# Performance work log

Hardware: AMD Instinct MI355X
Metric: run time of the kernel (lower is better)

Reference implementation:

```python
import jax, jax.numpy as jnp
import numpy as np

B, T, D = 2, 2048, 2048
NH, NKV, HD = 16, 4, 128
EPS = 1e-6
ROPE_THETA = 10000.0


def rms_norm(x, w):
    # per-head RMSNorm over the last (head_dim) axis
    var = jnp.mean(jnp.square(x), axis=-1, keepdims=True)
    return x * jax.lax.rsqrt(var + EPS) * w


def rope_sin_cos(seq_len, dim, dtype):
    inv_freq = 1.0 / (ROPE_THETA ** (jnp.arange(0, dim, 2, dtype=jnp.float32) / dim))
    t = jnp.arange(seq_len, dtype=jnp.float32)
    ang = jnp.outer(t, inv_freq)                      # [T, HD/2]
    ang = jnp.concatenate([ang, ang], axis=-1)         # [T, HD]
    return jnp.sin(ang).astype(dtype), jnp.cos(ang).astype(dtype)


def rotate_half(x):
    x1, x2 = jnp.split(x, 2, axis=-1)
    return jnp.concatenate([-x2, x1], axis=-1)


def apply_rope(x, sin, cos):
    # x: [B, T, H, HD]; sin/cos: [T, HD]
    s = sin[None, :, None, :]
    c = cos[None, :, None, :]
    return x * c + rotate_half(x) * s


def setup_inputs() -> dict:
    key = jax.random.key(0)
    ks = jax.random.split(key, 5)
    scale = 1.0 / np.sqrt(D)
    return {
        "x": jax.random.normal(ks[0], (B, T, D), jnp.float32),
        "wq": jax.random.normal(ks[1], (D, D), jnp.float32) * scale,
        "wk": jax.random.normal(ks[2], (NKV * HD, D), jnp.float32) * scale,
        "wv": jax.random.normal(ks[3], (NKV * HD, D), jnp.float32) * scale,
        "wo": jax.random.normal(ks[4], (D, D), jnp.float32) * scale,
        "q_norm_w": jnp.ones((HD,), jnp.float32),
        "k_norm_w": jnp.ones((HD,), jnp.float32),
    }


def reference(x, wq, wk, wv, wo, q_norm_w, k_norm_w):
    b, t, _ = x.shape
    q = (x @ wq.T).reshape(b, t, NH, HD)    # [B,T,NH,HD]
    k = (x @ wk.T).reshape(b, t, NKV, HD)   # [B,T,NKV,HD]
    v = (x @ wv.T).reshape(b, t, NKV, HD)

    # per-head QK RMS norm
    q = rms_norm(q, q_norm_w)
    k = rms_norm(k, k_norm_w)

    # RoPE
    sin, cos = rope_sin_cos(t, HD, x.dtype)
    q = apply_rope(q, sin, cos)
    k = apply_rope(k, sin, cos)

    # GQA: expand kv heads to match query heads
    rep = NH // NKV
    k = jnp.repeat(k, rep, axis=2)          # [B,T,NH,HD]
    v = jnp.repeat(v, rep, axis=2)

    # causal SDPA
    scale = 1.0 / np.sqrt(HD)
    scores = jnp.einsum('bqhd,bkhd->bhqk', q, k) * scale
    causal = jnp.tril(jnp.ones((t, t), bool))
    scores = jnp.where(causal[None, None], scores, jnp.finfo(scores.dtype).min)
    probs = jax.nn.softmax(scores, axis=-1)
    att = jnp.einsum('bhqk,bkhd->bqhd', probs, v).reshape(b, t, NH * HD)
    return att @ wo.T
```

## Files before the change

### kernel.cpp

```cpp
#include <hip/hip_runtime.h>
#include <hip/hip_bf16.h>

#define B_ 2
#define T_ 2048
#define D_ 2048
#define NH_ 16
#define NKV_ 4
#define HD_ 128

using bf16 = __bf16;
using bf16x8 = __attribute__((ext_vector_type(8))) __bf16;
using bf16x4 = __attribute__((ext_vector_type(4))) __bf16;
using f32x4 = __attribute__((ext_vector_type(4))) float;

__device__ __forceinline__ void gld_lds16(bf16* lds, const bf16* g) {
  __builtin_amdgcn_global_load_lds(
      (const __attribute__((address_space(1))) void*)g,
      (__attribute__((address_space(3))) void*)lds, 16, 0, 0);
}

__global__ __launch_bounds__(256) void cvt_bf16(const float* __restrict__ in,
                                                bf16* __restrict__ out, int n4) {
  int i = blockIdx.x * 256 + threadIdx.x;
  if (i >= n4) return;
  float4 v = ((const float4*)in)[i];
  bf16x4 o;
  o[0] = (bf16)v.x; o[1] = (bf16)v.y; o[2] = (bf16)v.z; o[3] = (bf16)v.w;
  ((bf16x4*)out)[i] = o;
}

template<typename OutT>
__global__ __launch_bounds__(256) void gemm_bt(const bf16* __restrict__ A,
                                               const bf16* __restrict__ Bt,
                                               OutT* __restrict__ C,
                                               int M, int N, int K) {
  __shared__ bf16 As[128 * 32];
  __shared__ bf16 Bs[128 * 32];
  const int tid = threadIdx.x;
  const int wid = tid >> 6;
  const int lane = tid & 63;
  const int g = lane >> 4, r = lane & 15;
  const int wm = wid >> 1, wn = wid & 1;
  const int gx = gridDim.x;
  const int nwg = gx * gridDim.y;
  const int flat = blockIdx.y * gx + blockIdx.x;
  const int swz = (flat & 7) * (nwg >> 3) + (flat >> 3);
  const long bm = (long)(swz / gx) * 128, bn = (long)(swz % gx) * 128;
  f32x4 acc[4][4] = {};

  for (int k0 = 0; k0 < K; k0 += 32) {
    __syncthreads();
    for (int c = 0; c < 2; ++c) {
      int ch = wid * 2 + c;
      int row = ch * 16 + (lane >> 2);
      int col = (lane & 3) * 8;
      gld_lds16(As + ch * 512, A + (bm + row) * K + k0 + col);
      gld_lds16(Bs + ch * 512, Bt + (bn + row) * K + k0 + col);
    }
    asm volatile("s_waitcnt vmcnt(0)" ::: "memory");
    __syncthreads();
    bf16x8 af[4], bfr[4];
    for (int m = 0; m < 4; ++m)
      af[m] = *(const bf16x8*)(As + (wm * 64 + m * 16 + r) * 32 + g * 8);
    for (int n = 0; n < 4; ++n)
      bfr[n] = *(const bf16x8*)(Bs + (wn * 64 + n * 16 + r) * 32 + g * 8);
    for (int m = 0; m < 4; ++m)
      for (int n = 0; n < 4; ++n)
        acc[m][n] = __builtin_amdgcn_mfma_f32_16x16x32_bf16(af[m], bfr[n], acc[m][n], 0, 0, 0);
  }

  for (int m = 0; m < 4; ++m)
    for (int n = 0; n < 4; ++n)
      for (int e = 0; e < 4; ++e) {
        long row = bm + wm * 64 + m * 16 + g * 4 + e;
        long col = bn + wn * 64 + n * 16 + r;
        C[row * N + col] = (OutT)acc[m][n][e];
      }
}

template<int IS_K>
__global__ __launch_bounds__(256) void norm_rope(const bf16* __restrict__ qkv,
                                                 const float* __restrict__ w,
                                                 bf16* __restrict__ out) {
  const int lane = threadIdx.x & 63;
  const int rloc = threadIdx.x >> 6;
  const int NHH = IS_K ? NKV_ : NH_;
  const int COFF = IS_K ? 2048 : 0;
  const long rid = (long)blockIdx.x * 4 + rloc;
  const int h = (int)(rid % NHH);
  const long bt = rid / NHH;
  const int t = (int)(bt % T_);
  const bf16* src = qkv + bt * 3072 + COFF + h * HD_;
  float v0 = (float)src[lane];
  float v1 = (float)src[lane + 64];
  float ss = v0 * v0 + v1 * v1;
  for (int o = 1; o < 64; o <<= 1) ss += __shfl_xor(ss, o, 64);
  float inv = rsqrtf(ss * (1.f / HD_) + 1e-6f);
  float n0 = v0 * inv * w[lane];
  float n1 = v1 * inv * w[lane + 64];
  float ang = (float)t * exp2f((float)lane * (-13.287712379549449f / 64.f));
  float sv, cv;
  __sincosf(ang, &sv, &cv);
  float o0 = n0 * cv - n1 * sv;
  float o1 = n1 * cv + n0 * sv;
  bf16* dst;
  if (IS_K) {
    long b = bt / T_;
    dst = out + ((b * NKV_ + h) * (long)T_ + t) * HD_;
  } else {
    dst = out + (bt * NH_ + h) * HD_;
  }
  dst[lane] = (bf16)o0;
  dst[lane + 64] = (bf16)o1;
}

__global__ __launch_bounds__(256) void vpack(const bf16* __restrict__ qkv,
                                             bf16* __restrict__ Vt) {
  __shared__ float tile[64][65];
  const int tt = blockIdx.x;
  const int dd = blockIdx.y & 1;
  const int bkv = blockIdx.y >> 1;
  const long b = bkv >> 2;
  const int kv = bkv & 3;
  const int t0 = tt * 64, d0 = dd * 64;
  for (int i = 0; i < 2; ++i) {
    int row = i * 32 + (threadIdx.x >> 3);
    int c8 = (threadIdx.x & 7) * 8;
    bf16x8 v = *(const bf16x8*)&qkv[(b * T_ + t0 + row) * 3072 + 2560 + kv * HD_ + d0 + c8];
    for (int j = 0; j < 8; ++j) tile[row][c8 + j] = (float)v[j];
  }
  __syncthreads();
  for (int i = 0; i < 2; ++i) {
    int drow = i * 32 + (threadIdx.x >> 3);
    int tc8 = (threadIdx.x & 7) * 8;
    bf16x8 o;
    for (int j = 0; j < 8; ++j) o[j] = (bf16)tile[tc8 + j][drow];
    *(bf16x8*)&Vt[((b * NKV_ + kv) * (long)HD_ + d0 + drow) * T_ + t0 + tc8] = o;
  }
}

__global__ __launch_bounds__(512) void flash_attn(const bf16* __restrict__ Q,
                                                  const bf16* __restrict__ K,
                                                  const bf16* __restrict__ V,
                                                  bf16* __restrict__ O) {
  __shared__ bf16 Ks[2][64 * 128];
  __shared__ bf16 Vs[2][128 * 64];
  __shared__ bf16 Ps[8][16 * 64];
  const int qt = (gridDim.x - 1) - blockIdx.x;
  const int h = blockIdx.y, b = blockIdx.z;
  const int kv = h >> 2;
  const int tid = threadIdx.x, wid = tid >> 6, lane = tid & 63;
  const int g = lane >> 4, r = lane & 15;
  const int q0 = qt * 128;
  const int qbase = q0 + wid * 16;
  const int q = qbase + r;

  bf16x8 aq[4];
  const bf16* qp = Q + ((long)(b * T_ + q)) * (NH_ * HD_) + h * HD_;
  for (int kk = 0; kk < 4; ++kk) aq[kk] = *(const bf16x8*)(qp + kk * 32 + g * 8);

  f32x4 oacc[8] = {};
  float m_run = -1e30f, l_run = 0.f;

  const bf16* Kbase = K + ((long)(b * NKV_ + kv)) * T_ * HD_;
  const bf16* Vbase = V + ((long)(b * NKV_ + kv)) * (long)HD_ * T_;
  const int nkt = 2 * qt + 2;

  auto stageKV = [&](int buf, int k0) {
    for (int c = 0; c < 2; ++c) {
      int ch = wid * 2 + c;
      {
        int row = ch * 4 + (lane >> 4);
        int srccol = ((lane & 15) ^ (row & 7)) * 8;
        gld_lds16(&Ks[buf][ch * 512], Kbase + (long)(k0 + row) * HD_ + srccol);
      }
      {
        int row = ch * 8 + (lane >> 3);
        int srccol = ((lane & 7) ^ (row & 7)) * 8;
        gld_lds16(&Vs[buf][ch * 512], Vbase + (long)row * T_ + k0 + srccol);
      }
    }
  };

  stageKV(0, 0);
  for (int kt = 0; kt < nkt; ++kt) {
    const int k0 = kt * 64;
    const int cur = kt & 1;
    if (kt + 1 < nkt) {
      stageKV(cur ^ 1, k0 + 64);
      asm volatile("s_waitcnt vmcnt(4)" ::: "memory");
    } else {
      asm volatile("s_waitcnt vmcnt(0)" ::: "memory");
    }
    __builtin_amdgcn_s_barrier();

    f32x4 s[4] = {};
    __builtin_amdgcn_s_setprio(1);
    for (int n = 0; n < 4; ++n)
      for (int kk = 0; kk < 4; ++kk) {
        int row = n * 16 + r;
        bf16x8 bk = *(const bf16x8*)(&Ks[cur][row * 128 + (((kk * 4 + g) ^ (row & 7)) * 8)]);
        s[n] = __builtin_amdgcn_mfma_f32_16x16x32_bf16(bk, aq[kk], s[n], 0, 0, 0);
      }
    __builtin_amdgcn_s_setprio(0);

    const float scale = 0.088388347648318447f;
    const bool domask = (k0 + 63 > qbase);
    float mx = -1e30f;
    if (domask) {
      for (int n = 0; n < 4; ++n) {
        const int km = k0 + n * 16 + g * 4;
        for (int e = 0; e < 4; ++e) {
          float v = s[n][e] * scale;
          if (km + e > q) v = -1e30f;
          s[n][e] = v;
          mx = fmaxf(mx, v);
        }
      }
    } else {
      for (int n = 0; n < 4; ++n)
        for (int e = 0; e < 4; ++e) {
          float v = s[n][e] * scale;
          s[n][e] = v;
          mx = fmaxf(mx, v);
        }
    }
    mx = fmaxf(mx, __shfl_xor(mx, 16, 64));
    mx = fmaxf(mx, __shfl_xor(mx, 32, 64));
    float mnew = fmaxf(m_run, mx);
    float alpha = __expf(m_run - mnew);
    float ls = 0.f;
    for (int n = 0; n < 4; ++n) {
      bf16x4 pb;
      for (int e = 0; e < 4; ++e) {
        float p = __expf(s[n][e] - mnew);
        ls += p;
        pb[e] = (bf16)p;
      }
      int c = n * 2 + (g >> 1);
      *(bf16x4*)(&Ps[wid][r * 64 + ((c ^ (r & 7)) * 8) + (g & 1) * 4]) = pb;
    }
    ls += __shfl_xor(ls, 16, 64);
    ls += __shfl_xor(ls, 32, 64);
    m_run = mnew;
    l_run = l_run * alpha + ls;

    float al[4];
    for (int e = 0; e < 4; ++e)
      al[e] = __shfl(alpha, (lane & 48) | (g * 4 + e), 64);
    for (int dt = 0; dt < 8; ++dt)
      for (int e = 0; e < 4; ++e) oacc[dt][e] *= al[e];

    asm volatile("s_waitcnt lgkmcnt(0)" ::: "memory");

    __builtin_amdgcn_s_setprio(1);
    for (int kk = 0; kk < 2; ++kk) {
      bf16x8 ap = *(const bf16x8*)(&Ps[wid][r * 64 + (((kk * 4 + g) ^ (r & 7)) * 8)]);
      for (int dt = 0; dt < 8; ++dt) {
        int row = dt * 16 + r;
        bf16x8 bv = *(const bf16x8*)(&Vs[cur][row * 64 + (((kk * 4 + g) ^ (row & 7)) * 8)]);
        oacc[dt] = __builtin_amdgcn_mfma_f32_16x16x32_bf16(ap, bv, oacc[dt], 0, 0, 0);
      }
    }
    __builtin_amdgcn_s_setprio(0);
    __builtin_amdgcn_s_barrier();
  }

  float li[4];
  for (int e = 0; e < 4; ++e) {
    float lv = __shfl(l_run, (lane & 48) | (g * 4 + e), 64);
    li[e] = 1.f / lv;
  }
  for (int e = 0; e < 4; ++e) {
    const int grow = q0 + wid * 16 + g * 4 + e;
    bf16* dst = O + ((long)(b * T_ + grow)) * (NH_ * HD_) + h * HD_;
    for (int dt = 0; dt < 8; ++dt)
      dst[dt * 16 + r] = (bf16)(oacc[dt][e] * li[e]);
  }
}

extern "C" void kernel_launch(void* const* d_in, const int* in_sizes, int n_in,
                              void* d_out, int out_size, void* d_ws, size_t ws_size,
                              hipStream_t stream) {
  const float* x  = (const float*)d_in[0];
  const float* wq = (const float*)d_in[1];
  const float* wk = (const float*)d_in[2];
  const float* wv = (const float*)d_in[3];
  const float* wo = (const float*)d_in[4];
  const float* qw = (const float*)d_in[5];
  const float* kw = (const float*)d_in[6];
  float* out = (float*)d_out;

  char* p = (char*)d_ws;
  bf16* xb    = (bf16*)(p);
  bf16* wqkvb = (bf16*)(p + 16777216);
  bf16* wob   = (bf16*)(p + 29360128);
  bf16* QKVr  = (bf16*)(p + 37748736);
  bf16* Qb    = (bf16*)(p + 62914560);
  bf16* Kb    = (bf16*)(p + 79691776);
  bf16* Vt    = (bf16*)(p + 83886080);
  bf16* attb  = (bf16*)(p + 88080384);

  cvt_bf16<<<8192, 256, 0, stream>>>(x,  xb, 2097152);
  cvt_bf16<<<4096, 256, 0, stream>>>(wq, wqkvb,           1048576);
  cvt_bf16<<<1024, 256, 0, stream>>>(wk, wqkvb + 4194304,  262144);
  cvt_bf16<<<1024, 256, 0, stream>>>(wv, wqkvb + 5242880,  262144);
  cvt_bf16<<<4096, 256, 0, stream>>>(wo, wob, 1048576);

  gemm_bt<bf16><<<dim3(24, 32), 256, 0, stream>>>(xb, wqkvb, QKVr, 4096, 3072, 2048);

  norm_rope<0><<<16384, 256, 0, stream>>>(QKVr, qw, Qb);
  norm_rope<1><<<4096, 256, 0, stream>>>(QKVr, kw, Kb);
  vpack<<<dim3(32, 16), 256, 0, stream>>>(QKVr, Vt);

  flash_attn<<<dim3(16, 16, 2), 512, 0, stream>>>(Qb, Kb, Vt, attb);

  gemm_bt<float><<<dim3(16, 32), 256, 0, stream>>>(attb, wob, out, 4096, 2048, 2048);
}
```

Measured before the change: 256.1 us.

## Use exp2 softmax with lazy rescale and prefetch V fragments in flash attention

Folds log2(e) into the score scale so the softmax uses exp2f. Rescaling of the output accumulator is skipped unless some row max grows by more than 8 (in log2 units), which removes most of the per-tile multiplies. The first half of the V fragments is loaded from LDS before the softmax math so those reads overlap with the ALU work, and launch bounds now request 4 waves per SIMD. The cost is extra registers held across the softmax and possible spills under the tighter register bound, plus slightly larger intermediate exponent values from the lazy max.

```diff
diff --git a/kernel.cpp b/kernel.cpp
--- a/kernel.cpp
+++ b/kernel.cpp
@@ -139,10 +139,10 @@
   }
 }
 
-__global__ __launch_bounds__(512) void flash_attn(const bf16* __restrict__ Q,
-                                                  const bf16* __restrict__ K,
-                                                  const bf16* __restrict__ V,
-                                                  bf16* __restrict__ O) {
+__global__ __launch_bounds__(512, 4) void flash_attn(const bf16* __restrict__ Q,
+                                                     const bf16* __restrict__ K,
+                                                     const bf16* __restrict__ V,
+                                                     bf16* __restrict__ O) {
   __shared__ bf16 Ks[2][64 * 128];
   __shared__ bf16 Vs[2][128 * 64];
   __shared__ bf16 Ps[8][16 * 64];
@@ -204,14 +204,21 @@
       }
     __builtin_amdgcn_s_setprio(0);
 
-    const float scale = 0.088388347648318447f;
+    bf16x8 bva[8];
+    for (int dt = 0; dt < 8; ++dt) {
+      int row = dt * 16 + r;
+      bva[dt] = *(const bf16x8*)(&Vs[cur][row * 64 + ((g ^ (row & 7)) * 8)]);
+    }
+    __builtin_amdgcn_sched_barrier(0);
+
+    const float scale2 = 0.12751743f;
     const bool domask = (k0 + 63 > qbase);
     float mx = -1e30f;
     if (domask) {
       for (int n = 0; n < 4; ++n) {
         const int km = k0 + n * 16 + g * 4;
         for (int e = 0; e < 4; ++e) {
-          float v = s[n][e] * scale;
+          float v = s[n][e] * scale2;
           if (km + e > q) v = -1e30f;
           s[n][e] = v;
           mx = fmaxf(mx, v);
@@ -220,20 +227,20 @@
     } else {
       for (int n = 0; n < 4; ++n)
         for (int e = 0; e < 4; ++e) {
-          float v = s[n][e] * scale;
+          float v = s[n][e] * scale2;
           s[n][e] = v;
           mx = fmaxf(mx, v);
         }
     }
     mx = fmaxf(mx, __shfl_xor(mx, 16, 64));
     mx = fmaxf(mx, __shfl_xor(mx, 32, 64));
-    float mnew = fmaxf(m_run, mx);
-    float alpha = __expf(m_run - mnew);
+    const bool resc = !__all(mx <= m_run + 8.f);
+    const float mnew = resc ? fmaxf(m_run, mx) : m_run;
     float ls = 0.f;
     for (int n = 0; n < 4; ++n) {
       bf16x4 pb;
       for (int e = 0; e < 4; ++e) {
-        float p = __expf(s[n][e] - mnew);
+        float p = exp2f(s[n][e] - mnew);
         ls += p;
         pb[e] = (bf16)p;
       }
@@ -242,25 +249,34 @@
     }
     ls += __shfl_xor(ls, 16, 64);
     ls += __shfl_xor(ls, 32, 64);
-    m_run = mnew;
-    l_run = l_run * alpha + ls;
-
-    float al[4];
-    for (int e = 0; e < 4; ++e)
-      al[e] = __shfl(alpha, (lane & 48) | (g * 4 + e), 64);
-    for (int dt = 0; dt < 8; ++dt)
-      for (int e = 0; e < 4; ++e) oacc[dt][e] *= al[e];
+    if (resc) {
+      float alpha = exp2f(m_run - mnew);
+      float al[4];
+      for (int e = 0; e < 4; ++e)
+        al[e] = __shfl(alpha, (lane & 48) | (g * 4 + e), 64);
+      for (int dt = 0; dt < 8; ++dt)
+        for (int e = 0; e < 4; ++e) oacc[dt][e] *= al[e];
+      l_run = l_run * alpha + ls;
+      m_run = mnew;
+    } else {
+      l_run += ls;
+    }
 
     asm volatile("s_waitcnt lgkmcnt(0)" ::: "memory");
 
     __builtin_amdgcn_s_setprio(1);
-    for (int kk = 0; kk < 2; ++kk) {
-      bf16x8 ap = *(const bf16x8*)(&Ps[wid][r * 64 + (((kk * 4 + g) ^ (r & 7)) * 8)]);
+    {
+      bf16x8 ap0 = *(const bf16x8*)(&Ps[wid][r * 64 + ((g ^ (r & 7)) * 8)]);
+      bf16x8 bvb[8];
       for (int dt = 0; dt < 8; ++dt) {
         int row = dt * 16 + r;
-        bf16x8 bv = *(const bf16x8*)(&Vs[cur][row * 64 + (((kk * 4 + g) ^ (row & 7)) * 8)]);
-        oacc[dt] = __builtin_amdgcn_mfma_f32_16x16x32_bf16(ap, bv, oacc[dt], 0, 0, 0);
-      }
+        bvb[dt] = *(const bf16x8*)(&Vs[cur][row * 64 + (((4 + g) ^ (row & 7)) * 8)]);
+      }
+      bf16x8 ap1 = *(const bf16x8*)(&Ps[wid][r * 64 + (((4 + g) ^ (r & 7)) * 8)]);
+      for (int dt = 0; dt < 8; ++dt)
+        oacc[dt] = __builtin_amdgcn_mfma_f32_16x16x32_bf16(ap0, bva[dt], oacc[dt], 0, 0, 0);
+      for (int dt = 0; dt < 8; ++dt)
+        oacc[dt] = __builtin_amdgcn_mfma_f32_16x16x32_bf16(ap1, bvb[dt], oacc[dt], 0, 0, 0);
     }
     __builtin_amdgcn_s_setprio(0);
     __builtin_amdgcn_s_barrier();
```

Result: slower. 339.9 us (+32.7%).
